# Kernel optimization log

Hardware: AMD Instinct MI355X
Metric: run time of the kernel (lower is better)

Reference implementation:

```python
import jax, jax.numpy as jnp
import numpy as np
import math

B, T, IN_DIM, HID = 64, 512, 1024, 1024
TAU_MEM = 20.0
ALPHA = math.exp(-1.0 / TAU_MEM)
THRESHOLD = 1.0


def setup_inputs() -> dict:
    key = jax.random.key(0)
    kx, kw, kb = jax.random.split(key, 3)
    s = 1.0 / math.sqrt(IN_DIM)  # torch Linear default init scale
    x = jax.random.normal(kx, (B, T, IN_DIM), dtype=jnp.float32)
    W = jax.random.uniform(kw, (HID, IN_DIM), minval=-s, maxval=s, dtype=jnp.float32)
    b = jax.random.uniform(kb, (HID,), minval=-s, maxval=s, dtype=jnp.float32)
    return {"x": x, "W": W, "b": b}


def reference(x, W, b):
    # Precompute the batched GEMM once: I[b,t,h] = fc(x[:,t])
    I = jnp.einsum("bti,hi->bth", x, W) + b  # [B,T,H]

    def step(mem, I_t):
        mem = ALPHA * mem + I_t                         # leaky integrate
        spike = (mem >= THRESHOLD).astype(mem.dtype)    # fire
        mem = mem * (1.0 - spike)                       # hard reset
        return mem, spike

    mem0 = jnp.zeros((x.shape[0], HID), dtype=x.dtype)
    mem_final, spikes_tbh = jax.lax.scan(step, mem0, jnp.swapaxes(I, 0, 1))
    spikes = jnp.swapaxes(spikes_tbh, 0, 1)  # [B,T,H]
    return spikes, mem_final
```

## Files before the change

### kernel.cpp

```cpp
#include <hip/hip_runtime.h>

#define B_    64
#define T_    512
#define KDIM  1024
#define HID_  1024

#define BM 64
#define BN 32
#define BK 16
#define LDA 20
#define NSL 64
#define BOFF 1280
#define BUFSZ 1920

#define ALPHA_F 0.95122942450071400909f

typedef float v4f __attribute__((ext_vector_type(4)));
typedef float v2f __attribute__((ext_vector_type(2)));

__global__ __launch_bounds__(128, 2) void snn_gemm_np(
    const float* __restrict__ x,
    const float* __restrict__ W,
    float* __restrict__ Iout)
{
#pragma clang fp contract(off)
    __shared__ float smem[2 * BUFSZ];
    float* const AB0 = smem;
    float* const AB1 = smem + BUFSZ;

    const int tid = threadIdx.x;
    const int bb  = blockIdx.x;
    const int t0  = blockIdx.y * BM;
    const int h0  = blockIdx.z * BN;

    const int tx = tid & 7;
    const int ty = tid >> 3;

    const int sr = tid >> 2;
    const int sc = (tid & 3) << 2;

    const float* xb = x + ((size_t)bb * T_ + t0) * KDIM;
    const float* Wb = W + (size_t)h0 * KDIM;

    float4 pa0, pa1, pw;
    pa0 = *(const float4*)&xb[(size_t)sr * KDIM + sc];
    pa1 = *(const float4*)&xb[(size_t)(32 + sr) * KDIM + sc];
    pw  = *(const float4*)&Wb[(size_t)sr * KDIM + sc];
    *(float4*)&AB0[sr * LDA + sc]        = pa0;
    *(float4*)&AB0[(32 + sr) * LDA + sc] = pa1;
    *(float4*)&AB0[BOFF + sr * LDA + sc] = pw;
    pa0 = *(const float4*)&xb[(size_t)sr * KDIM + 16 + sc];
    pa1 = *(const float4*)&xb[(size_t)(32 + sr) * KDIM + 16 + sc];
    pw  = *(const float4*)&Wb[(size_t)sr * KDIM + 16 + sc];
    __syncthreads();

    v2f p01[4][4], p23[4][4];
#pragma unroll
    for (int j = 0; j < 4; ++j)
#pragma unroll
        for (int i = 0; i < 4; ++i) {
            p01[j][i] = (v2f)(0.0f);
            p23[j][i] = (v2f)(0.0f);
        }

    for (int s = 0; s < NSL; ++s) {
        float* const cb = (s & 1) ? AB1 : AB0;
        float* const nb = (s & 1) ? AB0 : AB1;

        if (s + 1 < NSL) {
            *(float4*)&nb[sr * LDA + sc]        = pa0;
            *(float4*)&nb[(32 + sr) * LDA + sc] = pa1;
            *(float4*)&nb[BOFF + sr * LDA + sc] = pw;
        }
        if (s + 2 < NSL) {
            const int nk = (s + 2) << 4;
            pa0 = *(const float4*)&xb[(size_t)sr * KDIM + nk + sc];
            pa1 = *(const float4*)&xb[(size_t)(32 + sr) * KDIM + nk + sc];
            pw  = *(const float4*)&Wb[(size_t)sr * KDIM + nk + sc];
        }
#pragma unroll
        for (int q = 3; q >= 0; --q) {
            const int qc = q << 2;
            v2f a01[4], a23[4], b01[4], b23[4];
#pragma unroll
            for (int j = 0; j < 4; ++j) {
                const v4f a = *(const v4f*)&cb[(ty + 16 * j) * LDA + qc];
                a01[j] = a.xy; a23[j] = a.zw;
            }
#pragma unroll
            for (int i = 0; i < 4; ++i) {
                const v4f b = *(const v4f*)&cb[BOFF + (tx + 8 * i) * LDA + qc];
                b01[i] = b.xy; b23[i] = b.zw;
            }
#pragma unroll
            for (int j = 0; j < 4; ++j)
#pragma unroll
                for (int i = 0; i < 4; ++i) {
                    const v2f m01 = a01[j] * b01[i];
                    const v2f m23 = a23[j] * b23[i];
                    p01[j][i] = p01[j][i] + m01;
                    p23[j][i] = p23[j][i] + m23;
                }
        }
        __syncthreads();
    }

    float* const Ob = Iout + ((size_t)bb * T_ + t0) * HID_ + h0;
#pragma unroll
    for (int j = 0; j < 4; ++j)
#pragma unroll
        for (int i = 0; i < 4; ++i) {
            const float s01 = p01[j][i].x + p01[j][i].y;
            const float s23 = p23[j][i].x + p23[j][i].y;
            Ob[(ty + 16 * j) * HID_ + tx + 8 * i] = s01 + s23;
        }
}

__global__ __launch_bounds__(256, 2) void snn_scan(
    float* __restrict__ IS,
    const float* __restrict__ bias,
    float* __restrict__ memf)
{
#pragma clang fp contract(off)
    const int gid = blockIdx.x * 256 + threadIdx.x;
    const int b = gid >> 10;
    const int h = gid & (HID_ - 1);
    float* col = IS + (size_t)b * T_ * HID_ + h;
    const float bv = bias[h];
    float mem = 0.0f;

    float cur[16], nxt[16];
#pragma unroll
    for (int k = 0; k < 16; ++k) cur[k] = col[(size_t)k * HID_];

    for (int tg = 0; tg < T_; tg += 16) {
        if (tg + 16 < T_) {
#pragma unroll
            for (int k = 0; k < 16; ++k)
                nxt[k] = col[(size_t)(tg + 16 + k) * HID_];
        }
#pragma unroll
        for (int k = 0; k < 16; ++k) {
            const float It = cur[k] + bv;
            const float am = ALPHA_F * mem;
            mem = am + It;
            const bool fire = (mem >= 1.0f);
            col[(size_t)(tg + k) * HID_] = fire ? 1.0f : 0.0f;
            if (fire) mem = 0.0f;
        }
#pragma unroll
        for (int k = 0; k < 16; ++k) cur[k] = nxt[k];
    }
    memf[(size_t)b * HID_ + h] = mem;
}

extern "C" void kernel_launch(void* const* d_in, const int* in_sizes, int n_in,
                              void* d_out, int out_size, void* d_ws, size_t ws_size,
                              hipStream_t stream) {
    const float* x    = (const float*)d_in[0];
    const float* W    = (const float*)d_in[1];
    const float* bias = (const float*)d_in[2];
    float* out    = (float*)d_out;
    float* spikes = out;
    float* memf   = out + (size_t)B_ * T_ * HID_;

    dim3 g1(B_, T_ / BM, HID_ / BN);
    snn_gemm_np<<<g1, dim3(128), 0, stream>>>(x, W, spikes);

    snn_scan<<<dim3((B_ * HID_) / 256), dim3(256), 0, stream>>>(
        spikes, bias, memf);
}
```

Measured before the change: 1.579 ms.

## Triple-buffer GEMM shared tiles and prefetch next-slice register fragments

Moves the GEMM from double to triple LDS buffering, with global prefetch running three slices ahead. The first fragment of the next slice is loaded into registers before the barrier, so compute can start right after it. The A tile row stride drops from 20 to 16 floats, which shrinks the LDS footprint but may add bank conflicts on A fragment reads. The extra LDS per block and the added fragment registers could reduce occupancy.

Result: slower. 1.995 ms (+26.4%).

```diff
diff --git a/kernel.cpp b/kernel.cpp
--- a/kernel.cpp
+++ b/kernel.cpp
@@ -8,10 +8,11 @@
 #define BM 64
 #define BN 32
 #define BK 16
-#define LDA 20
+#define LDAA 16
+#define LDAB 20
 #define NSL 64
-#define BOFF 1280
-#define BUFSZ 1920
+#define BNOFF 1024
+#define BUFSZ 1664
 
 #define ALPHA_F 0.95122942450071400909f
 
@@ -24,9 +25,7 @@
     float* __restrict__ Iout)
 {
 #pragma clang fp contract(off)
-    __shared__ float smem[2 * BUFSZ];
-    float* const AB0 = smem;
-    float* const AB1 = smem + BUFSZ;
+    __shared__ float smem[3 * BUFSZ];
 
     const int tid = threadIdx.x;
     const int bb  = blockIdx.x;
@@ -42,16 +41,45 @@
     const float* xb = x + ((size_t)bb * T_ + t0) * KDIM;
     const float* Wb = W + (size_t)h0 * KDIM;
 
+#define LOADFRAG(AF, BF, BASE, QC)                                         \
+    {                                                                      \
+        _Pragma("unroll")                                                  \
+        for (int j = 0; j < 4; ++j)                                        \
+            AF[j] = *(const v4f*)&smem[(BASE) + (ty + 16 * j) * LDAA + (QC)]; \
+        _Pragma("unroll")                                                  \
+        for (int i = 0; i < 4; ++i)                                        \
+            BF[i] = *(const v4f*)&smem[(BASE) + BNOFF + (tx + 8 * i) * LDAB + (QC)]; \
+    }
+
+#define MACFRAG(AF, BF)                                                    \
+    {                                                                      \
+        _Pragma("unroll")                                                  \
+        for (int j = 0; j < 4; ++j)                                        \
+            _Pragma("unroll")                                              \
+            for (int i = 0; i < 4; ++i) {                                  \
+                const v2f m01 = AF[j].xy * BF[i].xy;                       \
+                const v2f m23 = AF[j].zw * BF[i].zw;                       \
+                p01[j][i] = p01[j][i] + m01;                               \
+                p23[j][i] = p23[j][i] + m23;                               \
+            }                                                              \
+    }
+
     float4 pa0, pa1, pw;
     pa0 = *(const float4*)&xb[(size_t)sr * KDIM + sc];
     pa1 = *(const float4*)&xb[(size_t)(32 + sr) * KDIM + sc];
     pw  = *(const float4*)&Wb[(size_t)sr * KDIM + sc];
-    *(float4*)&AB0[sr * LDA + sc]        = pa0;
-    *(float4*)&AB0[(32 + sr) * LDA + sc] = pa1;
-    *(float4*)&AB0[BOFF + sr * LDA + sc] = pw;
+    *(float4*)&smem[sr * LDAA + sc]            = pa0;
+    *(float4*)&smem[(32 + sr) * LDAA + sc]     = pa1;
+    *(float4*)&smem[BNOFF + sr * LDAB + sc]    = pw;
     pa0 = *(const float4*)&xb[(size_t)sr * KDIM + 16 + sc];
     pa1 = *(const float4*)&xb[(size_t)(32 + sr) * KDIM + 16 + sc];
     pw  = *(const float4*)&Wb[(size_t)sr * KDIM + 16 + sc];
+    *(float4*)&smem[BUFSZ + sr * LDAA + sc]         = pa0;
+    *(float4*)&smem[BUFSZ + (32 + sr) * LDAA + sc]  = pa1;
+    *(float4*)&smem[BUFSZ + BNOFF + sr * LDAB + sc] = pw;
+    pa0 = *(const float4*)&xb[(size_t)sr * KDIM + 32 + sc];
+    pa1 = *(const float4*)&xb[(size_t)(32 + sr) * KDIM + 32 + sc];
+    pw  = *(const float4*)&Wb[(size_t)sr * KDIM + 32 + sc];
     __syncthreads();
 
     v2f p01[4][4], p23[4][4];
@@ -63,46 +91,33 @@
             p23[j][i] = (v2f)(0.0f);
         }
 
+    v4f fa[4], fb[4];
+    LOADFRAG(fa, fb, 0, 12);
+
+    int cur = 0, pre = BUFSZ, wrt = 2 * BUFSZ;
+
     for (int s = 0; s < NSL; ++s) {
-        float* const cb = (s & 1) ? AB1 : AB0;
-        float* const nb = (s & 1) ? AB0 : AB1;
-
-        if (s + 1 < NSL) {
-            *(float4*)&nb[sr * LDA + sc]        = pa0;
-            *(float4*)&nb[(32 + sr) * LDA + sc] = pa1;
-            *(float4*)&nb[BOFF + sr * LDA + sc] = pw;
+        if (s + 2 < NSL) {
+            *(float4*)&smem[wrt + sr * LDAA + sc]         = pa0;
+            *(float4*)&smem[wrt + (32 + sr) * LDAA + sc]  = pa1;
+            *(float4*)&smem[wrt + BNOFF + sr * LDAB + sc] = pw;
         }
-        if (s + 2 < NSL) {
-            const int nk = (s + 2) << 4;
+        if (s + 3 < NSL) {
+            const int nk = (s + 3) << 4;
             pa0 = *(const float4*)&xb[(size_t)sr * KDIM + nk + sc];
             pa1 = *(const float4*)&xb[(size_t)(32 + sr) * KDIM + nk + sc];
             pw  = *(const float4*)&Wb[(size_t)sr * KDIM + nk + sc];
         }
-#pragma unroll
-        for (int q = 3; q >= 0; --q) {
-            const int qc = q << 2;
-            v2f a01[4], a23[4], b01[4], b23[4];
-#pragma unroll
-            for (int j = 0; j < 4; ++j) {
-                const v4f a = *(const v4f*)&cb[(ty + 16 * j) * LDA + qc];
-                a01[j] = a.xy; a23[j] = a.zw;
-            }
-#pragma unroll
-            for (int i = 0; i < 4; ++i) {
-                const v4f b = *(const v4f*)&cb[BOFF + (tx + 8 * i) * LDA + qc];
-                b01[i] = b.xy; b23[i] = b.zw;
-            }
-#pragma unroll
-            for (int j = 0; j < 4; ++j)
-#pragma unroll
-                for (int i = 0; i < 4; ++i) {
-                    const v2f m01 = a01[j] * b01[i];
-                    const v2f m23 = a23[j] * b23[i];
-                    p01[j][i] = p01[j][i] + m01;
-                    p23[j][i] = p23[j][i] + m23;
-                }
+        {
+            v4f ga[4], gb[4];
+            MACFRAG(fa, fb);
+            LOADFRAG(ga, gb, cur, 8);  MACFRAG(ga, gb);
+            LOADFRAG(ga, gb, cur, 4);  MACFRAG(ga, gb);
+            LOADFRAG(ga, gb, cur, 0);  MACFRAG(ga, gb);
         }
+        if (s + 1 < NSL) LOADFRAG(fa, fb, pre, 12);
         __syncthreads();
+        const int tmp = cur; cur = pre; pre = wrt; wrt = tmp;
     }
 
     float* const Ob = Iout + ((size_t)bb * T_ + t0) * HID_ + h0;
@@ -114,6 +129,8 @@
             const float s23 = p23[j][i].x + p23[j][i].y;
             Ob[(ty + 16 * j) * HID_ + tx + 8 * i] = s01 + s23;
         }
+#undef LOADFRAG
+#undef MACFRAG
 }
 
 __global__ __launch_bounds__(256, 2) void snn_scan(
```
